# Kernel tuning notes

Measured on AMD Instinct MI355X. Metric: run time of the kernel, lower is better.

## Reference

```python
import jax, jax.numpy as jnp
import numpy as np
import math

D_MODEL = 1024
N_HEADS = 16
D_K = D_MODEL // N_HEADS
THETA = 0.1


def setup_inputs() -> dict:
    key = jax.random.key(0)
    ks = jax.random.split(key, 6)
    scale = np.sqrt(1.0 / D_MODEL).astype(np.float32)
    x = jax.random.normal(ks[0], (4, 2048, D_MODEL), dtype=jnp.float32)
    W_q = jax.random.normal(ks[1], (D_MODEL, D_MODEL), dtype=jnp.float32) * scale
    W_k = jax.random.normal(ks[2], (D_MODEL, D_MODEL), dtype=jnp.float32) * scale
    W_v = jax.random.normal(ks[3], (D_MODEL, D_MODEL), dtype=jnp.float32) * scale
    W_o = jax.random.normal(ks[4], (D_MODEL, D_MODEL), dtype=jnp.float32) * scale
    alpha = jnp.ones((1,), dtype=jnp.float32)
    return {"x": x, "W_q": W_q, "W_k": W_k, "W_v": W_v, "W_o": W_o, "alpha": alpha}


def reference(x, W_q, W_k, W_v, W_o, alpha):
    B, S, _ = x.shape
    Q = x @ W_q
    K = x @ W_k
    V = x @ W_v
    # non-commutative elementwise transforms
    Q = Q + THETA * jnp.sin(Q)
    K = K + THETA * jnp.cos(K)
    V = V + alpha * THETA * jnp.tanh(V)
    # split heads: [B, H, S, d_k]
    def split(t):
        return t.reshape(B, S, N_HEADS, D_K).transpose(0, 2, 1, 3)
    Qh, Kh, Vh = split(Q), split(K), split(V)
    scores = jnp.einsum('bhqd,bhkd->bhqk', Qh, Kh) / math.sqrt(D_K)
    attn = jax.nn.softmax(scores, axis=-1)
    out = jnp.einsum('bhqk,bhkd->bhqd', attn, Vh)
    out = out.transpose(0, 2, 1, 3).reshape(B, S, D_MODEL)
    return out @ W_o
```

## Files before the change

### kernel.cpp

```cpp
#include <hip/hip_runtime.h>

typedef __bf16 bf16x8 __attribute__((ext_vector_type(8)));
typedef float f32x4 __attribute__((ext_vector_type(4)));
typedef float f32x16 __attribute__((ext_vector_type(16)));

#define MFMA16(a,b,c) __builtin_amdgcn_mfma_f32_16x16x32_bf16(a,b,c,0,0,0)
#define MFMA32(a,b,c) __builtin_amdgcn_mfma_f32_32x32x16_bf16(a,b,c,0,0,0)

__device__ __forceinline__ unsigned short f2bf(float f) {
  unsigned int u = __float_as_uint(f);
  u = (u + 0x7FFFu + ((u >> 16) & 1u)) >> 16;
  return (unsigned short)u;
}

__device__ __forceinline__ void gload16(const void* g, void* l) {
  __builtin_amdgcn_global_load_lds(
      (const __attribute__((address_space(1))) void*)g,
      (__attribute__((address_space(3))) void*)l, 16, 0, 0);
}

__device__ __forceinline__ float vexp2(float x) {
  float r;
  asm("v_exp_f32 %0, %1" : "=v"(r) : "v"(x));
  return r;
}

__device__ __forceinline__ bf16x8 mk_pfrag(int hi, float p0, float p1, float p2, float p3,
                                           float p4, float p5, float p6, float p7) {
  unsigned int a0, a1, b0, b1;
  asm("v_cvt_pk_bf16_f32 %0, %1, %2" : "=v"(a0) : "v"(p0), "v"(p1));
  asm("v_cvt_pk_bf16_f32 %0, %1, %2" : "=v"(a1) : "v"(p2), "v"(p3));
  asm("v_cvt_pk_bf16_f32 %0, %1, %2" : "=v"(b0) : "v"(p4), "v"(p5));
  asm("v_cvt_pk_bf16_f32 %0, %1, %2" : "=v"(b1) : "v"(p6), "v"(p7));
  unsigned int x = __shfl_xor(hi ? a0 : b0, 32);
  unsigned int y = __shfl_xor(hi ? a1 : b1, 32);
  uint4 w;
  w.x = hi ? x : a0;
  w.y = hi ? y : a1;
  w.z = hi ? b0 : x;
  w.w = hi ? b1 : y;
  return *reinterpret_cast<bf16x8*>(&w);
}

__global__ __launch_bounds__(256) void k_convx(const float* __restrict__ x,
                                               unsigned short* __restrict__ xb) {
  int i = (blockIdx.x * 256 + threadIdx.x) * 4;
  float4 v = *reinterpret_cast<const float4*>(x + i);
  ushort4 o;
  o.x = f2bf(v.x); o.y = f2bf(v.y); o.z = f2bf(v.z); o.w = f2bf(v.w);
  *reinterpret_cast<ushort4*>(xb + i) = o;
}

__global__ __launch_bounds__(256) void k_transw(const float* __restrict__ W,
                                                unsigned short* __restrict__ WT) {
  __shared__ float t[32][33];
  int bx = blockIdx.x * 32;
  int by = blockIdx.y * 32;
  int tx = threadIdx.x & 31;
  int ty = threadIdx.x >> 5;
#pragma unroll
  for (int i = 0; i < 32; i += 8)
    t[ty + i][tx] = W[(size_t)(by + ty + i) * 1024 + bx + tx];
  __syncthreads();
#pragma unroll
  for (int i = 0; i < 32; i += 8)
    WT[(size_t)(bx + ty + i) * 1024 + by + tx] = f2bf(t[tx][ty + i]);
}

template <int EPI>
__global__ __launch_bounds__(256) void k_gemm(
    const unsigned short* __restrict__ A, const unsigned short* __restrict__ BT, int K,
    unsigned short* __restrict__ Qf, unsigned short* __restrict__ Kf,
    unsigned short* __restrict__ Vf, const float* __restrict__ alphaPtr,
    float* __restrict__ Out) {
  __shared__ __align__(16) unsigned short smem[128 * 136];
  unsigned short* AsBase = smem;
  unsigned short* BsBase = smem + 128 * 32;
  const int tid = threadIdx.x;
  const int wave = tid >> 6, lane = tid & 63;
  const int l15 = lane & 15, lg = lane >> 4;
  const int wr = wave >> 1, wc = wave & 1;
  const int bm = blockIdx.x, bn = blockIdx.y;

  f32x4 acc[4][4] = {};
  const unsigned short* Ab = A + (size_t)bm * 128 * K;
  const unsigned short* Bb = BT + (size_t)bn * 128 * K;

  const int r0 = tid >> 2, q0 = (tid & 3) * 8;
  const int r1 = r0 + 64;
  char* ldsA = (char*)AsBase + wave * 1024;
  char* ldsB = (char*)BsBase + wave * 1024;

  for (int k0 = 0; k0 < K; k0 += 32) {
    gload16((const void*)(Ab + (size_t)r0 * K + k0 + q0), ldsA);
    gload16((const void*)(Ab + (size_t)r1 * K + k0 + q0), ldsA + 4096);
    gload16((const void*)(Bb + (size_t)r0 * K + k0 + q0), ldsB);
    gload16((const void*)(Bb + (size_t)r1 * K + k0 + q0), ldsB + 4096);
    __syncthreads();
    bf16x8 af[4], bfr[4];
#pragma unroll
    for (int mi = 0; mi < 4; ++mi)
      af[mi] = *reinterpret_cast<const bf16x8*>(&AsBase[(wr * 64 + mi * 16 + l15) * 32 + lg * 8]);
#pragma unroll
    for (int ni = 0; ni < 4; ++ni)
      bfr[ni] = *reinterpret_cast<const bf16x8*>(&BsBase[(wc * 64 + ni * 16 + l15) * 32 + lg * 8]);
#pragma unroll
    for (int mi = 0; mi < 4; ++mi)
#pragma unroll
      for (int ni = 0; ni < 4; ++ni)
        acc[mi][ni] = MFMA16(af[mi], bfr[ni], acc[mi][ni]);
    __syncthreads();
  }

  if (EPI == 0) {
    const float av = alphaPtr[0];
    const int t = bn >> 3;
#pragma unroll
    for (int mi = 0; mi < 4; ++mi)
#pragma unroll
      for (int ni = 0; ni < 4; ++ni)
#pragma unroll
        for (int r = 0; r < 4; ++r) {
          int row = wr * 64 + mi * 16 + lg * 4 + r;
          int col = wc * 64 + ni * 16 + l15;
          float v = acc[mi][ni][r];
          if (t == 0) v += 0.1f * __sinf(v);
          else if (t == 1) v += 0.1f * __cosf(v);
          else {
            float e = __expf(2.0f * v);
            v += av * 0.1f * (1.0f - 2.0f * __builtin_amdgcn_rcpf(e + 1.0f));
          }
          smem[row * 136 + col] = f2bf(v);
        }
    __syncthreads();
    unsigned short* dst = (t == 0) ? Qf : (t == 1) ? Kf : Vf;
    const int c16 = tid & 15, rb = tid >> 4;
    const int ncol0 = (bn & 7) * 128;
#pragma unroll
    for (int i2 = 0; i2 < 8; ++i2) {
      int srow = rb + i2 * 16;
      uint4 val = *reinterpret_cast<const uint4*>(&smem[srow * 136 + c16 * 8]);
      *reinterpret_cast<uint4*>(dst + (size_t)(bm * 128 + srow) * 1024 + ncol0 + c16 * 8) = val;
    }
  } else {
#pragma unroll
    for (int ni = 0; ni < 4; ++ni) {
      int n = bn * 128 + wc * 64 + ni * 16 + l15;
#pragma unroll
      for (int mi = 0; mi < 4; ++mi) {
        int row = bm * 128 + wr * 64 + mi * 16 + lg * 4;
#pragma unroll
        for (int r = 0; r < 4; ++r)
          Out[(size_t)(row + r) * 1024 + n] = acc[mi][ni][r];
      }
    }
  }
}

__global__ __launch_bounds__(256, 4) void k_attn(const unsigned short* __restrict__ Qf,
                                                 const unsigned short* __restrict__ Kf,
                                                 const unsigned short* __restrict__ Vf,
                                                 unsigned short* __restrict__ AO) {
  __shared__ __align__(16) unsigned short smem[2 * (4096 + 4608)];
  const int tid = threadIdx.x;
  const int wave = tid >> 6, lane = tid & 63;
  const int l31 = lane & 31, hi = lane >> 5;
  const int f = (blockIdx.y << 4) | blockIdx.x;
  const int nf = ((f & 7) << 7) | (f >> 3);
  const int qb = nf & 15, bh = nf >> 4;
  const int b = bh >> 4, h = bh & 15;

  const unsigned short* Qb = Qf + ((size_t)b * 2048 + qb * 128 + wave * 32) * 1024 + h * 64;
  const unsigned short* Kb = Kf + (size_t)b * 2048 * 1024 + h * 64;
  const unsigned short* Vb = Vf + (size_t)b * 2048 * 1024 + h * 64;

  bf16x8 qfr[4];
#pragma unroll
  for (int ds = 0; ds < 4; ++ds)
    qfr[ds] = *reinterpret_cast<const bf16x8*>(Qb + (size_t)l31 * 1024 + ds * 16 + hi * 8);

  float mrun = -1.0e30f, lsum = 0.f;
  f32x16 o0 = {}, o1 = {};

  const int krow0 = wave * 16 + (lane >> 3);
  const int ksrcc = ((lane & 7) ^ (lane >> 3)) << 3;
  const int kxor = l31 & 7;

  const int sr = tid >> 3, sc = (tid & 7) * 8;
  const int u8 = tid & 7;
  const int swz0 = (l31 >> 3) << 3;
  const int swz1 = ((l31 >> 3) ^ 4) << 3;

  const float C1 = 0.18033688011112042f;

  uint4 va0, va1;
  va0 = *reinterpret_cast<const uint4*>(Vb + (size_t)sr * 1024 + sc);
  va1 = *reinterpret_cast<const uint4*>(Vb + (size_t)(sr + 32) * 1024 + sc);

  {
    unsigned short* Ks = smem;
    unsigned short* VT = smem + 4096;
    gload16((const void*)(Kb + (size_t)krow0 * 1024 + ksrcc), (char*)Ks + wave * 2048);
    gload16((const void*)(Kb + (size_t)(krow0 + 8) * 1024 + ksrcc), (char*)Ks + wave * 2048 + 1024);
    unsigned int w0[4] = {va0.x, va0.y, va0.z, va0.w};
    unsigned int w1[4] = {va1.x, va1.y, va1.z, va1.w};
#pragma unroll
    for (int e = 0; e < 4; ++e) {
      int d = sc + 2 * e;
      VT[(d * 72 + sr) ^ (u8 << 3)] = (unsigned short)w0[e];
      VT[((d + 1) * 72 + sr) ^ (u8 << 3)] = (unsigned short)(w0[e] >> 16);
      VT[(d * 72 + sr + 32) ^ (u8 << 3)] = (unsigned short)w1[e];
      VT[((d + 1) * 72 + sr + 32) ^ (u8 << 3)] = (unsigned short)(w1[e] >> 16);
    }
  }
  __syncthreads();

  for (int t = 0; t < 32; ++t) {
    unsigned short* KsC = smem + (t & 1) * 8704;
    unsigned short* VTC = KsC + 4096;
    unsigned short* KsN = smem + ((t + 1) & 1) * 8704;
    unsigned short* VTN = KsN + 4096;

    if (t < 31) {
      int kn = (t + 1) * 64;
      gload16((const void*)(Kb + (size_t)(kn + krow0) * 1024 + ksrcc), (char*)KsN + wave * 2048);
      gload16((const void*)(Kb + (size_t)(kn + krow0 + 8) * 1024 + ksrcc),
              (char*)KsN + wave * 2048 + 1024);
      va0 = *reinterpret_cast<const uint4*>(Vb + (size_t)(kn + sr) * 1024 + sc);
      va1 = *reinterpret_cast<const uint4*>(Vb + (size_t)(kn + sr + 32) * 1024 + sc);
    }

    f32x16 s0 = {}, s1 = {};
    __builtin_amdgcn_s_setprio(1);
#pragma unroll
    for (int ds = 0; ds < 4; ++ds) {
      int ch = ((ds * 2 + hi) ^ kxor) * 8;
      bf16x8 kf0 = *reinterpret_cast<const bf16x8*>(&KsC[l31 * 64 + ch]);
      bf16x8 kf1 = *reinterpret_cast<const bf16x8*>(&KsC[(l31 + 32) * 64 + ch]);
      s0 = MFMA32(kf0, qfr[ds], s0);
      s1 = MFMA32(kf1, qfr[ds], s1);
    }
    __builtin_amdgcn_s_setprio(0);

    float pm0 = s0[0], pm1 = s0[1], pm2 = s0[2], pm3 = s0[3];
#pragma unroll
    for (int r = 4; r < 16; r += 4) {
      pm0 = fmaxf(pm0, s0[r]);     pm1 = fmaxf(pm1, s0[r + 1]);
      pm2 = fmaxf(pm2, s0[r + 2]); pm3 = fmaxf(pm3, s0[r + 3]);
    }
#pragma unroll
    for (int r = 0; r < 16; r += 4) {
      pm0 = fmaxf(pm0, s1[r]);     pm1 = fmaxf(pm1, s1[r + 1]);
      pm2 = fmaxf(pm2, s1[r + 2]); pm3 = fmaxf(pm3, s1[r + 3]);
    }
    float pmax = fmaxf(fmaxf(pm0, pm1), fmaxf(pm2, pm3));
    pmax = fmaxf(pmax, __shfl_xor(pmax, 32));

    if (!__all(pmax - mrun <= 64.0f)) {
      float mn = fmaxf(mrun, pmax);
      float corr = vexp2((mrun - mn) * C1);
      o0 *= corr; o1 *= corr; lsum *= corr;
      mrun = mn;
    }
    const float c2 = -mrun * C1;
    float rs0 = 0.f, rs1 = 0.f, rs2 = 0.f, rs3 = 0.f;
#pragma unroll
    for (int r = 0; r < 16; r += 4) {
      float p0 = vexp2(fmaf(s0[r], C1, c2));     s0[r] = p0;     rs0 += p0;
      float p1 = vexp2(fmaf(s0[r + 1], C1, c2)); s0[r + 1] = p1; rs1 += p1;
      float p2 = vexp2(fmaf(s0[r + 2], C1, c2)); s0[r + 2] = p2; rs2 += p2;
      float p3 = vexp2(fmaf(s0[r + 3], C1, c2)); s0[r + 3] = p3; rs3 += p3;
    }
#pragma unroll
    for (int r = 0; r < 16; r += 4) {
      float p0 = vexp2(fmaf(s1[r], C1, c2));     s1[r] = p0;     rs0 += p0;
      float p1 = vexp2(fmaf(s1[r + 1], C1, c2)); s1[r + 1] = p1; rs1 += p1;
      float p2 = vexp2(fmaf(s1[r + 2], C1, c2)); s1[r + 2] = p2; rs2 += p2;
      float p3 = vexp2(fmaf(s1[r + 3], C1, c2)); s1[r + 3] = p3; rs3 += p3;
    }
    float rsum = (rs0 + rs1) + (rs2 + rs3);
    rsum += __shfl_xor(rsum, 32);
    lsum += rsum;

    if (t < 31) {
      unsigned int w0[4] = {va0.x, va0.y, va0.z, va0.w};
      unsigned int w1[4] = {va1.x, va1.y, va1.z, va1.w};
#pragma unroll
      for (int e = 0; e < 4; ++e) {
        int d = sc + 2 * e;
        VTN[(d * 72 + sr) ^ (u8 << 3)] = (unsigned short)w0[e];
        VTN[((d + 1) * 72 + sr) ^ (u8 << 3)] = (unsigned short)(w0[e] >> 16);
        VTN[(d * 72 + sr + 32) ^ (u8 << 3)] = (unsigned short)w1[e];
        VTN[((d + 1) * 72 + sr + 32) ^ (u8 << 3)] = (unsigned short)(w1[e] >> 16);
      }
    }

    __builtin_amdgcn_s_setprio(1);
#pragma unroll
    for (int ks = 0; ks < 4; ++ks) {
      bf16x8 pf =
          (ks == 0) ? mk_pfrag(hi, s0[0], s0[1], s0[2], s0[3], s0[4], s0[5], s0[6], s0[7])
        : (ks == 1) ? mk_pfrag(hi, s0[8], s0[9], s0[10], s0[11], s0[12], s0[13], s0[14], s0[15])
        : (ks == 2) ? mk_pfrag(hi, s1[0], s1[1], s1[2], s1[3], s1[4], s1[5], s1[6], s1[7])
                    : mk_pfrag(hi, s1[8], s1[9], s1[10], s1[11], s1[12], s1[13], s1[14], s1[15]);
      bf16x8 v0 = *reinterpret_cast<const bf16x8*>(&VTC[(l31 * 72 + ks * 16 + hi * 8) ^ swz0]);
      bf16x8 v1 = *reinterpret_cast<const bf16x8*>(&VTC[((l31 + 32) * 72 + ks * 16 + hi * 8) ^ swz1]);
      o0 = MFMA32(v0, pf, o0);
      o1 = MFMA32(v1, pf, o1);
    }
    __builtin_amdgcn_s_setprio(0);
    __syncthreads();
  }

  const float inv = 1.0f / lsum;
  unsigned short* OL = smem + wave * 2304;
#pragma unroll
  for (int r = 0; r < 16; ++r) {
    int d0 = (r & 3) + 8 * (r >> 2) + 4 * hi;
    OL[l31 * 72 + d0] = f2bf(o0[r] * inv);
    OL[l31 * 72 + 32 + d0] = f2bf(o1[r] * inv);
  }
  __syncthreads();
#pragma unroll
  for (int p = 0; p < 4; ++p) {
    int u = tid + p * 256;
    int row = u >> 3, ch = u & 7;
    uint4 val = *reinterpret_cast<const uint4*>(&smem[(row >> 5) * 2304 + (row & 31) * 72 + ch * 8]);
    *reinterpret_cast<uint4*>(AO + ((size_t)b * 2048 + qb * 128 + row) * 1024 + h * 64 + ch * 8) = val;
  }
}

extern "C" void kernel_launch(void* const* d_in, const int* in_sizes, int n_in,
                              void* d_out, int out_size, void* d_ws, size_t ws_size,
                              hipStream_t stream) {
  const float* x = (const float*)d_in[0];
  const float* Wq = (const float*)d_in[1];
  const float* Wk = (const float*)d_in[2];
  const float* Wv = (const float*)d_in[3];
  const float* Wo = (const float*)d_in[4];
  const float* alpha = (const float*)d_in[5];
  float* out = (float*)d_out;

  char* ws = (char*)d_ws;
  unsigned short* xb  = (unsigned short*)(ws);
  unsigned short* WT3 = (unsigned short*)(ws + 16777216);
  unsigned short* WoT = (unsigned short*)(ws + 23068672);
  unsigned short* Qf  = (unsigned short*)(ws + 25165824);
  unsigned short* Kf  = (unsigned short*)(ws + 41943040);
  unsigned short* Vf  = (unsigned short*)(ws + 58720256);
  unsigned short* AO  = (unsigned short*)(ws + 75497472);

  k_convx<<<dim3(8192), dim3(256), 0, stream>>>(x, xb);
  k_transw<<<dim3(32, 32), dim3(256), 0, stream>>>(Wq, WT3);
  k_transw<<<dim3(32, 32), dim3(256), 0, stream>>>(Wk, WT3 + 1024 * 1024);
  k_transw<<<dim3(32, 32), dim3(256), 0, stream>>>(Wv, WT3 + 2 * 1024 * 1024);
  k_transw<<<dim3(32, 32), dim3(256), 0, stream>>>(Wo, WoT);

  k_gemm<0><<<dim3(64, 24), dim3(256), 0, stream>>>(xb, WT3, 1024, Qf, Kf, Vf, alpha, nullptr);
  k_attn<<<dim3(16, 64), dim3(256), 0, stream>>>(Qf, Kf, Vf, AO);
  k_gemm<1><<<dim3(64, 8), dim3(256), 0, stream>>>(AO, WoT, 1024, nullptr, nullptr, nullptr, nullptr, out);
}
```

Baseline: 234.7 us.

## Rewrite QKV projection GEMM with 256x256 tiles, double buffering and swizzled LDS

Replaces the templated QKV GEMM with a dedicated 512-thread kernel using 256x256 output tiles and a 64-wide K step. It double-buffers the global-to-LDS loads so the next tile loads while MFMAs run, and XOR-swizzles the LDS layout to avoid bank conflicts. It also raises wave priority around the MFMA blocks. The aim is more data reuse per LDS load and overlap of memory with compute, at the cost of large LDS use (one block per CU) and a grid of 384 blocks that may leave a partial wave.

```diff
diff --git a/kernel.cpp b/kernel.cpp
--- a/kernel.cpp
+++ b/kernel.cpp
@@ -67,11 +67,121 @@
     WT[(size_t)(bx + ty + i) * 1024 + by + tx] = f2bf(t[tx][ty + i]);
 }
 
-template <int EPI>
-__global__ __launch_bounds__(256) void k_gemm(
+__global__ __launch_bounds__(512, 2) void k_gemm2(
+    const unsigned short* __restrict__ A, const unsigned short* __restrict__ BT,
+    unsigned short* __restrict__ Qf, unsigned short* __restrict__ Kf,
+    unsigned short* __restrict__ Vf, const float* __restrict__ alphaPtr) {
+  __shared__ __align__(16) unsigned short smem[65536];
+  const int tid = threadIdx.x;
+  const int wave = tid >> 6, lane = tid & 63;
+  const int l15 = lane & 15, lg = lane >> 4;
+  const int wr = wave >> 2;
+  const int wc = wave & 3;
+  const int bm = blockIdx.x, bn = blockIdx.y;
+  const int K = 1024;
+
+  const unsigned short* Ab = A + (size_t)bm * 256 * K;
+  const unsigned short* Bb = BT + (size_t)bn * 256 * K;
+
+  const int srow = wave * 8 + (lane >> 3);
+  const int scol = ((lane & 7) ^ (lane >> 3)) * 8;
+
+  const int ck0 = ((lg) ^ (l15 & 7)) * 8;
+  const int ck1 = ((4 + lg) ^ (l15 & 7)) * 8;
+
+  f32x4 acc[8][4] = {};
+
+#pragma unroll
+  for (int h = 0; h < 2; ++h)
+#pragma unroll
+    for (int g = 0; g < 2; ++g) {
+      int R = h * 128 + g * 64 + srow;
+      int d = h * 8192 + g * 4096 + wave * 512;
+      gload16(Ab + (size_t)R * K + scol, (char*)smem + d * 2);
+      gload16(Bb + (size_t)R * K + scol, (char*)(smem + 16384) + d * 2);
+    }
+  __syncthreads();
+
+  for (int t = 0; t < 16; ++t) {
+    unsigned short* cur = smem + (t & 1) * 32768;
+    unsigned short* nxt = smem + ((t + 1) & 1) * 32768;
+
+    if (t < 15) {
+      int k0 = (t + 1) * 64;
+#pragma unroll
+      for (int h = 0; h < 2; ++h)
+#pragma unroll
+        for (int g = 0; g < 2; ++g) {
+          int R = h * 128 + g * 64 + srow;
+          int d = h * 8192 + g * 4096 + wave * 512;
+          gload16(Ab + (size_t)R * K + k0 + scol, (char*)nxt + d * 2);
+          gload16(Bb + (size_t)R * K + k0 + scol, (char*)(nxt + 16384) + d * 2);
+        }
+    }
+
+    bf16x8 bfr[4][2];
+#pragma unroll
+    for (int ni = 0; ni < 4; ++ni) {
+      int R = wc * 64 + ni * 16 + l15;
+      bfr[ni][0] = *reinterpret_cast<const bf16x8*>(&cur[16384 + R * 64 + ck0]);
+      bfr[ni][1] = *reinterpret_cast<const bf16x8*>(&cur[16384 + R * 64 + ck1]);
+    }
+
+#pragma unroll
+    for (int q = 0; q < 4; ++q) {
+      bf16x8 af[2][2];
+#pragma unroll
+      for (int i = 0; i < 2; ++i) {
+        int R = wr * 128 + (q * 2 + i) * 16 + l15;
+        af[i][0] = *reinterpret_cast<const bf16x8*>(&cur[R * 64 + ck0]);
+        af[i][1] = *reinterpret_cast<const bf16x8*>(&cur[R * 64 + ck1]);
+      }
+      __builtin_amdgcn_s_setprio(1);
+#pragma unroll
+      for (int i = 0; i < 2; ++i)
+#pragma unroll
+        for (int ni = 0; ni < 4; ++ni) {
+          acc[q * 2 + i][ni] = MFMA16(af[i][0], bfr[ni][0], acc[q * 2 + i][ni]);
+          acc[q * 2 + i][ni] = MFMA16(af[i][1], bfr[ni][1], acc[q * 2 + i][ni]);
+        }
+      __builtin_amdgcn_s_setprio(0);
+    }
+    __syncthreads();
+  }
+
+  const float av = alphaPtr[0];
+  const int t3 = bn >> 2;
+#pragma unroll
+  for (int mi = 0; mi < 8; ++mi)
+#pragma unroll
+    for (int ni = 0; ni < 4; ++ni)
+#pragma unroll
+      for (int r = 0; r < 4; ++r) {
+        int row = wr * 128 + mi * 16 + lg * 4 + r;
+        int col = wc * 64 + ni * 16 + l15;
+        float v = acc[mi][ni][r];
+        if (t3 == 0) v += 0.1f * __sinf(v);
+        else if (t3 == 1) v += 0.1f * __cosf(v);
+        else {
+          float e = __expf(2.0f * v);
+          v += av * 0.1f * (1.0f - 2.0f * __builtin_amdgcn_rcpf(e + 1.0f));
+        }
+        smem[row * 256 + (col ^ ((row & 7) << 3))] = f2bf(v);
+      }
+  __syncthreads();
+  unsigned short* dst = (t3 == 0) ? Qf : (t3 == 1) ? Kf : Vf;
+  const int ncol0 = (bn & 3) * 256;
+  const int er = tid >> 1;
+#pragma unroll
+  for (int i = 0; i < 16; ++i) {
+    int c = ((tid & 1) * 16 + i) * 8;
+    uint4 val = *reinterpret_cast<const uint4*>(&smem[er * 256 + (c ^ ((er & 7) << 3))]);
+    *reinterpret_cast<uint4*>(dst + (size_t)(bm * 256 + er) * 1024 + ncol0 + c) = val;
+  }
+}
+
+__global__ __launch_bounds__(256) void k_gemm1(
     const unsigned short* __restrict__ A, const unsigned short* __restrict__ BT, int K,
-    unsigned short* __restrict__ Qf, unsigned short* __restrict__ Kf,
-    unsigned short* __restrict__ Vf, const float* __restrict__ alphaPtr,
     float* __restrict__ Out) {
   __shared__ __align__(16) unsigned short smem[128 * 136];
   unsigned short* AsBase = smem;
@@ -112,47 +222,15 @@
     __syncthreads();
   }
 
-  if (EPI == 0) {
-    const float av = alphaPtr[0];
-    const int t = bn >> 3;
-#pragma unroll
-    for (int mi = 0; mi < 4; ++mi)
-#pragma unroll
-      for (int ni = 0; ni < 4; ++ni)
-#pragma unroll
-        for (int r = 0; r < 4; ++r) {
-          int row = wr * 64 + mi * 16 + lg * 4 + r;
-          int col = wc * 64 + ni * 16 + l15;
-          float v = acc[mi][ni][r];
-          if (t == 0) v += 0.1f * __sinf(v);
-          else if (t == 1) v += 0.1f * __cosf(v);
-          else {
-            float e = __expf(2.0f * v);
-            v += av * 0.1f * (1.0f - 2.0f * __builtin_amdgcn_rcpf(e + 1.0f));
-          }
-          smem[row * 136 + col] = f2bf(v);
-        }
-    __syncthreads();
-    unsigned short* dst = (t == 0) ? Qf : (t == 1) ? Kf : Vf;
-    const int c16 = tid & 15, rb = tid >> 4;
-    const int ncol0 = (bn & 7) * 128;
-#pragma unroll
-    for (int i2 = 0; i2 < 8; ++i2) {
-      int srow = rb + i2 * 16;
-      uint4 val = *reinterpret_cast<const uint4*>(&smem[srow * 136 + c16 * 8]);
-      *reinterpret_cast<uint4*>(dst + (size_t)(bm * 128 + srow) * 1024 + ncol0 + c16 * 8) = val;
-    }
-  } else {
-#pragma unroll
-    for (int ni = 0; ni < 4; ++ni) {
-      int n = bn * 128 + wc * 64 + ni * 16 + l15;
-#pragma unroll
-      for (int mi = 0; mi < 4; ++mi) {
-        int row = bm * 128 + wr * 64 + mi * 16 + lg * 4;
-#pragma unroll
-        for (int r = 0; r < 4; ++r)
-          Out[(size_t)(row + r) * 1024 + n] = acc[mi][ni][r];
-      }
+#pragma unroll
+  for (int ni = 0; ni < 4; ++ni) {
+    int n = bn * 128 + wc * 64 + ni * 16 + l15;
+#pragma unroll
+    for (int mi = 0; mi < 4; ++mi) {
+      int row = bm * 128 + wr * 64 + mi * 16 + lg * 4;
+#pragma unroll
+      for (int r = 0; r < 4; ++r)
+        Out[(size_t)(row + r) * 1024 + n] = acc[mi][ni][r];
     }
   }
 }
@@ -356,7 +434,7 @@
   k_transw<<<dim3(32, 32), dim3(256), 0, stream>>>(Wv, WT3 + 2 * 1024 * 1024);
   k_transw<<<dim3(32, 32), dim3(256), 0, stream>>>(Wo, WoT);
 
-  k_gemm<0><<<dim3(64, 24), dim3(256), 0, stream>>>(xb, WT3, 1024, Qf, Kf, Vf, alpha, nullptr);
+  k_gemm2<<<dim3(32, 12), dim3(512), 0, stream>>>(xb, WT3, Qf, Kf, Vf, alpha);
   k_attn<<<dim3(16, 64), dim3(256), 0, stream>>>(Qf, Kf, Vf, AO);
-  k_gemm<1><<<dim3(64, 8), dim3(256), 0, stream>>>(AO, WoT, 1024, nullptr, nullptr, nullptr, nullptr, out);
-}
+  k_gemm1<<<dim3(64, 8), dim3(256), 0, stream>>>(AO, WoT, 1024, out);
+}
```

Result: slower. 240.3 us (+2.4%).
